# Kernel optimization log

Hardware: AMD Instinct MI355X
Metric: run time of the kernel (lower is better)

The kernel has to match this reference:

```python
import jax, jax.numpy as jnp
import numpy as np

NUM_EMBEDDINGS = 1024
EMBEDDING_DIM = 256

def setup_inputs() -> dict:
    key = jax.random.key(0)
    k1, k2 = jax.random.split(key)
    x = jax.random.normal(k1, (8, 16, 32, 32, EMBEDDING_DIM), dtype=jnp.float32)
    embeddings = jax.random.normal(k2, (NUM_EMBEDDINGS, EMBEDDING_DIM), dtype=jnp.float32)
    return {"x": x, "embeddings": embeddings}

def reference(x, embeddings):
    # Flatten all leading dims to tokens: [N, D]
    flat = x.reshape(-1, EMBEDDING_DIM)
    # Squared euclidean distances via ||a||^2 + ||b||^2 - 2 a.b  -> [N, K]
    sim = jnp.matmul(flat, embeddings.T)
    distances = (jnp.sum(flat * flat, axis=1, keepdims=True)
                 + jnp.sum(embeddings * embeddings, axis=1)
                 - 2.0 * sim)
    encoding_indices = jnp.argmin(distances, axis=1)  # [N]
    quantized = embeddings[encoding_indices].reshape(x.shape)
    # Perplexity from code usage histogram (mean of one-hot == normalized counts)
    counts = jnp.zeros((NUM_EMBEDDINGS,), dtype=jnp.float32).at[encoding_indices].add(1.0)
    avg_probs = counts / flat.shape[0]
    perplexity = jnp.exp(-jnp.sum(avg_probs * jnp.log(avg_probs + 1e-10)))
    return quantized, perplexity
```

## Files before the change

kernel.cpp:

```cpp
#include <hip/hip_runtime.h>
#include <math.h>
#include <stdint.h>

#define NTOK 131072
#define DIM  256
#define KEMB 1024

typedef _Float16 f16x8 __attribute__((ext_vector_type(8)));
typedef float    f32x4 __attribute__((ext_vector_type(4)));

#define FLAG_CAP 65536
#define FLAG_THR 8u

static __device__ __forceinline__ unsigned umin32(unsigned a, unsigned b){ return a<b?a:b; }
static __device__ __forceinline__ unsigned umax32(unsigned a, unsigned b){ return a>b?a:b; }

static __device__ __forceinline__ void gload_lds16(const void* g, void* l) {
    __builtin_amdgcn_global_load_lds(
        (const __attribute__((address_space(1))) unsigned int*)g,
        (__attribute__((address_space(3))) unsigned int*)l, 16, 0, 0);
}

static __device__ __forceinline__ void split_hl(const float4& f0, const float4& f1,
                                                f16x8& h, f16x8& l) {
    float v[8] = {f0.x, f0.y, f0.z, f0.w, f1.x, f1.y, f1.z, f1.w};
    #pragma unroll
    for (int e = 0; e < 8; ++e) {
        const _Float16 hi = (_Float16)v[e];
        h[e] = hi;
        l[e] = (_Float16)(v[e] - (float)hi);
    }
}

__global__ __launch_bounds__(64) void prep_kernel(const float* __restrict__ emb,
                                                  float* __restrict__ eNorm,
                                                  float* __restrict__ cst2,
                                                  unsigned* __restrict__ counts,
                                                  unsigned* __restrict__ flagCnt,
                                                  _Float16* __restrict__ img_hi,
                                                  _Float16* __restrict__ img_lo) {
    const int k = blockIdx.x;
    const int lane = threadIdx.x;
    const float4 v = *reinterpret_cast<const float4*>(emb + (size_t)k * DIM + lane * 4);
    float s = v.x * v.x + v.y * v.y + v.z * v.z + v.w * v.w;
    #pragma unroll
    for (int m = 32; m; m >>= 1) s += __shfl_xor(s, m, 64);
    if (lane == 0) {
        eNorm[k] = s;
        cst2[k]  = s + 512.0f;
        counts[k] = 0u;
        if (k == 0) *flagCnt = 0u;
    }
    if (lane < 32) {
        const int p = lane;
        const int sl = p ^ (k & 7);
        const float4 f0 = *reinterpret_cast<const float4*>(emb + (size_t)k * DIM + sl * 8);
        const float4 f1 = *reinterpret_cast<const float4*>(emb + (size_t)k * DIM + sl * 8 + 4);
        f16x8 h, l;
        split_hl(f0, f1, h, l);
        *reinterpret_cast<f16x8*>(img_hi + (size_t)k * 256 + p * 8) = h;
        *reinterpret_cast<f16x8*>(img_lo + (size_t)k * 256 + p * 8) = l;
    }
}

__global__ __launch_bounds__(256, 4) void vq_main(const float* __restrict__ x,
                                                  const float* __restrict__ emb,
                                                  const _Float16* __restrict__ img,
                                                  const float* __restrict__ cst2,
                                                  int* __restrict__ idxArr,
                                                  unsigned* __restrict__ counts,
                                                  unsigned* __restrict__ flagCnt,
                                                  unsigned* __restrict__ flagList,
                                                  float* __restrict__ out) {
    __shared__ _Float16 B[2][8192];
    __shared__ float cst_s[1024];
    __shared__ int idx_s[128];

    const int tid  = threadIdx.x;
    const int wv   = tid >> 6;
    const int lane = tid & 63;
    const int g    = lane >> 4;
    const int c    = lane & 15;
    const int T0   = blockIdx.x * 128;
    const int T0w  = T0 + wv * 32;

    *reinterpret_cast<float4*>(&cst_s[tid * 4]) =
        *reinterpret_cast<const float4*>(&cst2[tid * 4]);

    #pragma unroll
    for (int i = 0; i < 4; ++i)
        gload_lds16((const char*)img + (i * 256 + tid) * 16,
                    (char*)&B[0][0] + i * 4096 + wv * 1024);

    f16x8 a[2][8];
    #pragma unroll
    for (int i = 0; i < 2; ++i) {
        const float* xr = x + (size_t)(T0w + i * 16 + c) * DIM + g * 8;
        #pragma unroll
        for (int kk = 0; kk < 8; ++kk) {
            const float4 f0 = *reinterpret_cast<const float4*>(xr + kk * 32);
            const float4 f1 = *reinterpret_cast<const float4*>(xr + kk * 32 + 4);
            a[i][kk] = (f16x8){(_Float16)f0.x, (_Float16)f0.y, (_Float16)f0.z, (_Float16)f0.w,
                               (_Float16)f1.x, (_Float16)f1.y, (_Float16)f1.z, (_Float16)f1.w};
        }
    }

    unsigned m1[8], m2[8];
    #pragma unroll
    for (int t = 0; t < 8; ++t) { m1[t] = 0xFFFFFFFFu; m2[t] = 0xFFFFFFFFu; }

    __syncthreads();

    for (int ec = 0; ec < 32; ++ec) {
        if (ec < 31) {
            const char* src = (const char*)img + (ec + 1) * 16384;
            char* dst = (char*)&B[(ec + 1) & 1][0];
            #pragma unroll
            for (int i = 0; i < 4; ++i)
                gload_lds16(src + (i * 256 + tid) * 16, dst + i * 4096 + wv * 1024);
        }

        const _Float16* Bc = &B[ec & 1][0];
        f32x4 acc[2][2];
        #pragma unroll
        for (int i = 0; i < 2; ++i)
            #pragma unroll
            for (int j = 0; j < 2; ++j) acc[i][j] = (f32x4){0.f, 0.f, 0.f, 0.f};

        #pragma unroll
        for (int kk = 0; kk < 8; ++kk) {
            f16x8 b[2];
            #pragma unroll
            for (int j = 0; j < 2; ++j) {
                const int row = j * 16 + c;
                const int s   = kk * 4 + g;
                b[j] = *reinterpret_cast<const f16x8*>(&Bc[row * 256 + ((s ^ (row & 7)) << 3)]);
            }
            #pragma unroll
            for (int i = 0; i < 2; ++i)
                #pragma unroll
                for (int j = 0; j < 2; ++j)
                    acc[i][j] = __builtin_amdgcn_mfma_f32_16x16x32_f16(a[i][kk], b[j], acc[i][j], 0, 0, 0);
        }

        #pragma unroll
        for (int j = 0; j < 2; ++j) {
            const int   col = ec * 32 + j * 16 + c;
            const float cst = cst_s[col];
            #pragma unroll
            for (int i = 0; i < 2; ++i)
                #pragma unroll
                for (int e = 0; e < 4; ++e) {
                    const float    d   = fmaf(acc[i][j][e], -2.0f, cst);
                    const unsigned key = (__builtin_bit_cast(unsigned, d) & 0xFFFFFC00u) | (unsigned)col;
                    const int t = i * 4 + e;
                    m2[t] = umin32(m2[t], umax32(key, m1[t]));
                    m1[t] = umin32(m1[t], key);
                }
        }
        __syncthreads();
    }

    #pragma unroll
    for (int off = 1; off < 16; off <<= 1) {
        #pragma unroll
        for (int t = 0; t < 8; ++t) {
            const unsigned o1 = __shfl_xor(m1[t], off, 64);
            const unsigned o2 = __shfl_xor(m2[t], off, 64);
            const unsigned nm2 = umin32(umin32(m2[t], o2), umax32(m1[t], o1));
            m1[t] = umin32(m1[t], o1);
            m2[t] = nm2;
        }
    }

    if (c == 0) {
        #pragma unroll
        for (int t = 0; t < 8; ++t) {
            const int row = (t >> 2) * 16 + g * 4 + (t & 3);
            const int idx = (int)(m1[t] & 1023u);
            idx_s[wv * 32 + row] = idx;
            idxArr[T0w + row] = idx;
            atomicAdd(&counts[idx], 1u);
            if (((m2[t] >> 10) - (m1[t] >> 10)) < FLAG_THR) {
                const unsigned pos = atomicAdd(flagCnt, 1u);
                if (pos < FLAG_CAP) flagList[pos] = (unsigned)(T0w + row);
            }
        }
    }
    __syncthreads();

    #pragma unroll 4
    for (int s = 0; s < 32; ++s) {
        const int fi  = s * 256 + tid;
        const int row = fi >> 6;
        const int q4  = fi & 63;
        const int em  = idx_s[row];
        *reinterpret_cast<float4*>(out + (size_t)(T0 + row) * DIM + q4 * 4) =
            *reinterpret_cast<const float4*>(emb + (size_t)em * DIM + q4 * 4);
    }
}

__global__ __launch_bounds__(256) void fixup_refine(const float* __restrict__ x,
                                                    const _Float16* __restrict__ img_hi,
                                                    const _Float16* __restrict__ img_lo,
                                                    const float* __restrict__ cst2,
                                                    const unsigned* __restrict__ flagCnt,
                                                    const unsigned* __restrict__ flagList,
                                                    uint2* __restrict__ refTop) {
    __shared__ _Float16 Bh[16384];
    __shared__ _Float16 Bl[16384];
    __shared__ float cst_s[1024];

    const unsigned nf = umin32(*flagCnt, (unsigned)FLAG_CAP);
    if (blockIdx.x * 64u >= nf) return;

    const int tid  = threadIdx.x;
    const int wv   = tid >> 6;
    const int lane = tid & 63;
    const int g    = lane >> 4;
    const int c    = lane & 15;
    const unsigned base = (blockIdx.x * 4u + (unsigned)wv) * 16u;

    *reinterpret_cast<float4*>(&cst_s[tid * 4]) =
        *reinterpret_cast<const float4*>(&cst2[tid * 4]);

    const unsigned myTok = flagList[(base + c) < nf ? (base + c) : 0];
    f16x8 ah[8], al[8];
    {
        const float* xr = x + (size_t)myTok * DIM + g * 8;
        #pragma unroll
        for (int kk = 0; kk < 8; ++kk) {
            const float4 f0 = *reinterpret_cast<const float4*>(xr + kk * 32);
            const float4 f1 = *reinterpret_cast<const float4*>(xr + kk * 32 + 4);
            split_hl(f0, f1, ah[kk], al[kk]);
        }
    }

    unsigned m1[4], m2[4];
    #pragma unroll
    for (int e = 0; e < 4; ++e) { m1[e] = 0xFFFFFFFFu; m2[e] = 0xFFFFFFFFu; }

    for (int ec = 0; ec < 16; ++ec) {
        __syncthreads();
        #pragma unroll
        for (int i = 0; i < 8; ++i) {
            gload_lds16((const char*)img_hi + ec * 32768 + (i * 256 + tid) * 16,
                        (char*)&Bh[0] + i * 4096 + wv * 1024);
            gload_lds16((const char*)img_lo + ec * 32768 + (i * 256 + tid) * 16,
                        (char*)&Bl[0] + i * 4096 + wv * 1024);
        }
        __syncthreads();

        f32x4 acc[4];
        #pragma unroll
        for (int j = 0; j < 4; ++j) acc[j] = (f32x4){0.f, 0.f, 0.f, 0.f};

        #pragma unroll
        for (int kk = 0; kk < 8; ++kk) {
            #pragma unroll
            for (int j = 0; j < 4; ++j) {
                const int row = j * 16 + c;
                const int off = row * 256 + (((kk * 4 + g) ^ (row & 7)) << 3);
                const f16x8 bh = *reinterpret_cast<const f16x8*>(&Bh[off]);
                const f16x8 bl = *reinterpret_cast<const f16x8*>(&Bl[off]);
                acc[j] = __builtin_amdgcn_mfma_f32_16x16x32_f16(ah[kk], bh, acc[j], 0, 0, 0);
                acc[j] = __builtin_amdgcn_mfma_f32_16x16x32_f16(ah[kk], bl, acc[j], 0, 0, 0);
                acc[j] = __builtin_amdgcn_mfma_f32_16x16x32_f16(al[kk], bh, acc[j], 0, 0, 0);
            }
        }

        #pragma unroll
        for (int j = 0; j < 4; ++j) {
            const int   col = ec * 64 + j * 16 + c;
            const float cst = cst_s[col];
            #pragma unroll
            for (int e = 0; e < 4; ++e) {
                const float    d   = fmaf(acc[j][e], -2.0f, cst);
                const unsigned key = (__builtin_bit_cast(unsigned, d) & 0xFFFFFC00u) | (unsigned)col;
                m2[e] = umin32(m2[e], umax32(key, m1[e]));
                m1[e] = umin32(m1[e], key);
            }
        }
    }

    #pragma unroll
    for (int off = 1; off < 16; off <<= 1) {
        #pragma unroll
        for (int e = 0; e < 4; ++e) {
            const unsigned o1 = __shfl_xor(m1[e], off, 64);
            const unsigned o2 = __shfl_xor(m2[e], off, 64);
            const unsigned nm2 = umin32(umin32(m2[e], o2), umax32(m1[e], o1));
            m1[e] = umin32(m1[e], o1);
            m2[e] = nm2;
        }
    }

    if (c == 0) {
        #pragma unroll
        for (int e = 0; e < 4; ++e) {
            const unsigned pos = base + (unsigned)(g * 4 + e);
            if (pos < nf) refTop[pos] = make_uint2(m1[e], m2[e]);
        }
    }
}

__global__ __launch_bounds__(256) void fixup_exact(const float* __restrict__ x,
                                                   const float* __restrict__ emb,
                                                   const float* __restrict__ eNorm,
                                                   const unsigned* __restrict__ flagCnt,
                                                   const unsigned* __restrict__ flagList,
                                                   const uint2* __restrict__ refTop,
                                                   int* __restrict__ idxArr,
                                                   unsigned* __restrict__ counts,
                                                   float* __restrict__ out) {
    const unsigned nf = umin32(*flagCnt, (unsigned)FLAG_CAP);
    const int tid  = threadIdx.x;
    const int wv   = tid >> 6;
    const int lane = tid & 63;

    for (unsigned pos = blockIdx.x * 4u + (unsigned)wv; pos < nf; pos += gridDim.x * 4u) {
        const unsigned tok = flagList[pos];
        const uint2 tk = refTop[pos];
        const int e1 = (int)(tk.x & 1023u);
        const int e2 = (int)(tk.y & 1023u);

        const float4 xv = *reinterpret_cast<const float4*>(x   + (size_t)tok * DIM + lane * 4);
        const float4 v1 = *reinterpret_cast<const float4*>(emb + (size_t)e1  * DIM + lane * 4);
        const float4 v2 = *reinterpret_cast<const float4*>(emb + (size_t)e2  * DIM + lane * 4);
        float p1 = xv.x * v1.x + xv.y * v1.y + xv.z * v1.z + xv.w * v1.w;
        float p2 = xv.x * v2.x + xv.y * v2.y + xv.z * v2.z + xv.w * v2.w;
        #pragma unroll
        for (int off = 1; off < 64; off <<= 1) {
            p1 += __shfl_xor(p1, off, 64);
            p2 += __shfl_xor(p2, off, 64);
        }
        const float d1 = eNorm[e1] - 2.0f * p1;
        const float d2 = eNorm[e2] - 2.0f * p2;
        const bool pick2 = (d2 < d1) || (d2 == d1 && e2 < e1);
        const int  ni   = pick2 ? e2 : e1;
        const int  old  = idxArr[tok];
        if (ni != old) {
            if (lane == 0) {
                idxArr[tok] = ni;
                atomicSub(&counts[old], 1u);
                atomicAdd(&counts[ni], 1u);
            }
            const float4 nv = pick2 ? v2 : v1;
            *reinterpret_cast<float4*>(out + (size_t)tok * DIM + lane * 4) = nv;
        }
    }
}

__global__ __launch_bounds__(256) void perp_kernel(const unsigned* __restrict__ counts,
                                                   float* __restrict__ out_perp) {
    __shared__ float red[256];
    const int tid = threadIdx.x;
    float s = 0.0f;
    for (int i = tid; i < KEMB; i += 256) {
        const float p = (float)counts[i] / (float)NTOK;
        s += p * logf(p + 1e-10f);
    }
    red[tid] = s;
    __syncthreads();
    for (int off = 128; off; off >>= 1) {
        if (tid < off) red[tid] += red[tid + off];
        __syncthreads();
    }
    if (tid == 0) *out_perp = expf(-red[0]);
}

extern "C" void kernel_launch(void* const* d_in, const int* in_sizes, int n_in,
                              void* d_out, int out_size, void* d_ws, size_t ws_size,
                              hipStream_t stream) {
    (void)in_sizes; (void)n_in; (void)out_size; (void)ws_size;
    const float* x   = (const float*)d_in[0];
    const float* emb = (const float*)d_in[1];
    float* out = (float*)d_out;

    char* ws = (char*)d_ws;
    float*     eNorm    = (float*)(ws);
    float*     cst2     = (float*)(ws + 4096);
    unsigned*  counts   = (unsigned*)(ws + 8192);
    unsigned*  flagCnt  = (unsigned*)(ws + 12288);
    unsigned*  flagList = (unsigned*)(ws + 16384);
    int*       idxArr   = (int*)(ws + 278528);
    _Float16*  img_hi   = (_Float16*)(ws + 802816);
    _Float16*  img_lo   = (_Float16*)(ws + 1327104);
    uint2*     refTop   = (uint2*)(ws + 1851392);

    prep_kernel<<<KEMB, 64, 0, stream>>>(emb, eNorm, cst2, counts, flagCnt, img_hi, img_lo);
    vq_main<<<NTOK / 128, 256, 0, stream>>>(x, emb, img_hi, cst2, idxArr, counts,
                                            flagCnt, flagList, out);
    fixup_refine<<<1024, 256, 0, stream>>>(x, img_hi, img_lo, cst2, flagCnt, flagList, refTop);
    fixup_exact<<<2048, 256, 0, stream>>>(x, emb, eNorm, flagCnt, flagList, refTop,
                                          idxArr, counts, out);
    perp_kernel<<<1, 256, 0, stream>>>(counts, out + (size_t)NTOK * DIM);
}
```

Measured before the change: 203.6 us.

## Drop LDS staging in vq_main; read codebook directly from global into registers

Removes the double-buffered LDS codebook tiles and the per-chunk barriers from the main VQ kernel. Each wave now holds 64 tokens of A fragments and streams 16 codebook rows per step straight from global/L2 memory. The launch bound drops to 2 blocks per SM to leave room for the larger register footprint, and each block now covers 256 tokens instead of 128. The prep kernel's swizzled image layout is dropped to match, so the codebook image is now row-major. This trades shared-memory reuse and synchronisation for reliance on L2 caching of the 512 KB fp16 codebook and more registers per thread, which may lower occupancy and raise load latency.

```diff
diff --git a/kernel.cpp b/kernel.cpp
--- a/kernel.cpp
+++ b/kernel.cpp
@@ -53,9 +53,8 @@
     }
     if (lane < 32) {
         const int p = lane;
-        const int sl = p ^ (k & 7);
-        const float4 f0 = *reinterpret_cast<const float4*>(emb + (size_t)k * DIM + sl * 8);
-        const float4 f1 = *reinterpret_cast<const float4*>(emb + (size_t)k * DIM + sl * 8 + 4);
+        const float4 f0 = *reinterpret_cast<const float4*>(emb + (size_t)k * DIM + p * 8);
+        const float4 f1 = *reinterpret_cast<const float4*>(emb + (size_t)k * DIM + p * 8 + 4);
         f16x8 h, l;
         split_hl(f0, f1, h, l);
         *reinterpret_cast<f16x8*>(img_hi + (size_t)k * 256 + p * 8) = h;
@@ -63,7 +62,7 @@
     }
 }
 
-__global__ __launch_bounds__(256, 4) void vq_main(const float* __restrict__ x,
+__global__ __launch_bounds__(256, 2) void vq_main(const float* __restrict__ x,
                                                   const float* __restrict__ emb,
                                                   const _Float16* __restrict__ img,
                                                   const float* __restrict__ cst2,
@@ -72,29 +71,19 @@
                                                   unsigned* __restrict__ flagCnt,
                                                   unsigned* __restrict__ flagList,
                                                   float* __restrict__ out) {
-    __shared__ _Float16 B[2][8192];
-    __shared__ float cst_s[1024];
-    __shared__ int idx_s[128];
+    __shared__ int idx_s[256];
 
     const int tid  = threadIdx.x;
     const int wv   = tid >> 6;
     const int lane = tid & 63;
     const int g    = lane >> 4;
     const int c    = lane & 15;
-    const int T0   = blockIdx.x * 128;
-    const int T0w  = T0 + wv * 32;
-
-    *reinterpret_cast<float4*>(&cst_s[tid * 4]) =
-        *reinterpret_cast<const float4*>(&cst2[tid * 4]);
-
-    #pragma unroll
-    for (int i = 0; i < 4; ++i)
-        gload_lds16((const char*)img + (i * 256 + tid) * 16,
-                    (char*)&B[0][0] + i * 4096 + wv * 1024);
-
-    f16x8 a[2][8];
-    #pragma unroll
-    for (int i = 0; i < 2; ++i) {
+    const int T0   = blockIdx.x * 256;
+    const int T0w  = T0 + wv * 64;
+
+    f16x8 a[4][8];
+    #pragma unroll
+    for (int i = 0; i < 4; ++i) {
         const float* xr = x + (size_t)(T0w + i * 16 + c) * DIM + g * 8;
         #pragma unroll
         for (int kk = 0; kk < 8; ++kk) {
@@ -105,66 +94,47 @@
         }
     }
 
-    unsigned m1[8], m2[8];
-    #pragma unroll
-    for (int t = 0; t < 8; ++t) { m1[t] = 0xFFFFFFFFu; m2[t] = 0xFFFFFFFFu; }
-
-    __syncthreads();
-
-    for (int ec = 0; ec < 32; ++ec) {
-        if (ec < 31) {
-            const char* src = (const char*)img + (ec + 1) * 16384;
-            char* dst = (char*)&B[(ec + 1) & 1][0];
+    unsigned m1[16], m2[16];
+    #pragma unroll
+    for (int t = 0; t < 16; ++t) { m1[t] = 0xFFFFFFFFu; m2[t] = 0xFFFFFFFFu; }
+
+    #pragma unroll 2
+    for (int ec = 0; ec < 64; ++ec) {
+        const int col = ec * 16 + c;
+        const float cst = cst2[col];
+
+        f16x8 b[8];
+        #pragma unroll
+        for (int kk = 0; kk < 8; ++kk)
+            b[kk] = *reinterpret_cast<const f16x8*>(
+                img + (size_t)col * 256 + (kk * 4 + g) * 8);
+
+        f32x4 acc[4];
+        #pragma unroll
+        for (int i = 0; i < 4; ++i) acc[i] = (f32x4){0.f, 0.f, 0.f, 0.f};
+
+        #pragma unroll
+        for (int kk = 0; kk < 8; ++kk)
             #pragma unroll
             for (int i = 0; i < 4; ++i)
-                gload_lds16(src + (i * 256 + tid) * 16, dst + i * 4096 + wv * 1024);
-        }
-
-        const _Float16* Bc = &B[ec & 1][0];
-        f32x4 acc[2][2];
-        #pragma unroll
-        for (int i = 0; i < 2; ++i)
+                acc[i] = __builtin_amdgcn_mfma_f32_16x16x32_f16(a[i][kk], b[kk], acc[i], 0, 0, 0);
+
+        #pragma unroll
+        for (int i = 0; i < 4; ++i)
             #pragma unroll
-            for (int j = 0; j < 2; ++j) acc[i][j] = (f32x4){0.f, 0.f, 0.f, 0.f};
-
-        #pragma unroll
-        for (int kk = 0; kk < 8; ++kk) {
-            f16x8 b[2];
-            #pragma unroll
-            for (int j = 0; j < 2; ++j) {
-                const int row = j * 16 + c;
-                const int s   = kk * 4 + g;
-                b[j] = *reinterpret_cast<const f16x8*>(&Bc[row * 256 + ((s ^ (row & 7)) << 3)]);
-            }
-            #pragma unroll
-            for (int i = 0; i < 2; ++i)
-                #pragma unroll
-                for (int j = 0; j < 2; ++j)
-                    acc[i][j] = __builtin_amdgcn_mfma_f32_16x16x32_f16(a[i][kk], b[j], acc[i][j], 0, 0, 0);
-        }
-
-        #pragma unroll
-        for (int j = 0; j < 2; ++j) {
-            const int   col = ec * 32 + j * 16 + c;
-            const float cst = cst_s[col];
-            #pragma unroll
-            for (int i = 0; i < 2; ++i)
-                #pragma unroll
-                for (int e = 0; e < 4; ++e) {
-                    const float    d   = fmaf(acc[i][j][e], -2.0f, cst);
-                    const unsigned key = (__builtin_bit_cast(unsigned, d) & 0xFFFFFC00u) | (unsigned)col;
-                    const int t = i * 4 + e;
-                    m2[t] = umin32(m2[t], umax32(key, m1[t]));
-                    m1[t] = umin32(m1[t], key);
-                }
-        }
-        __syncthreads();
+            for (int e = 0; e < 4; ++e) {
+                const float    d   = fmaf(acc[i][e], -2.0f, cst);
+                const unsigned key = (__builtin_bit_cast(unsigned, d) & 0xFFFFFC00u) | (unsigned)col;
+                const int t = i * 4 + e;
+                m2[t] = umin32(m2[t], umax32(key, m1[t]));
+                m1[t] = umin32(m1[t], key);
+            }
     }
 
     #pragma unroll
     for (int off = 1; off < 16; off <<= 1) {
         #pragma unroll
-        for (int t = 0; t < 8; ++t) {
+        for (int t = 0; t < 16; ++t) {
             const unsigned o1 = __shfl_xor(m1[t], off, 64);
             const unsigned o2 = __shfl_xor(m2[t], off, 64);
             const unsigned nm2 = umin32(umin32(m2[t], o2), umax32(m1[t], o1));
@@ -175,10 +145,12 @@
 
     if (c == 0) {
         #pragma unroll
-        for (int t = 0; t < 8; ++t) {
-            const int row = (t >> 2) * 16 + g * 4 + (t & 3);
+        for (int t = 0; t < 16; ++t) {
+            const int i   = t >> 2;
+            const int e   = t & 3;
+            const int row = i * 16 + g * 4 + e;
             const int idx = (int)(m1[t] & 1023u);
-            idx_s[wv * 32 + row] = idx;
+            idx_s[wv * 64 + row] = idx;
             idxArr[T0w + row] = idx;
             atomicAdd(&counts[idx], 1u);
             if (((m2[t] >> 10) - (m1[t] >> 10)) < FLAG_THR) {
@@ -190,7 +162,7 @@
     __syncthreads();
 
     #pragma unroll 4
-    for (int s = 0; s < 32; ++s) {
+    for (int s = 0; s < 64; ++s) {
         const int fi  = s * 256 + tid;
         const int row = fi >> 6;
         const int q4  = fi & 63;
@@ -260,7 +232,7 @@
             #pragma unroll
             for (int j = 0; j < 4; ++j) {
                 const int row = j * 16 + c;
-                const int off = row * 256 + (((kk * 4 + g) ^ (row & 7)) << 3);
+                const int off = row * 256 + (kk * 4 + g) * 8;
                 const f16x8 bh = *reinterpret_cast<const f16x8*>(&Bh[off]);
                 const f16x8 bl = *reinterpret_cast<const f16x8*>(&Bl[off]);
                 acc[j] = __builtin_amdgcn_mfma_f32_16x16x32_f16(ah[kk], bh, acc[j], 0, 0, 0);
@@ -389,7 +361,7 @@
     uint2*     refTop   = (uint2*)(ws + 1851392);
 
     prep_kernel<<<KEMB, 64, 0, stream>>>(emb, eNorm, cst2, counts, flagCnt, img_hi, img_lo);
-    vq_main<<<NTOK / 128, 256, 0, stream>>>(x, emb, img_hi, cst2, idxArr, counts,
+    vq_main<<<NTOK / 256, 256, 0, stream>>>(x, emb, img_hi, cst2, idxArr, counts,
                                             flagCnt, flagList, out);
     fixup_refine<<<1024, 256, 0, stream>>>(x, img_hi, img_lo, cst2, flagCnt, flagList, refTop);
     fixup_exact<<<2048, 256, 0, stream>>>(x, emb, eNorm, flagCnt, flagList, refTop,
```

New measurement: 317.3 us. 1.56x slower.
